# Kernel optimization log

Measured on AMD Instinct MI355X. Metric: run time of the kernel, lower is better.

Reference implementation:

```python
import jax, jax.numpy as jnp
import numpy as np

NUM_HEADS = 16

def _rope(t, cos, sin):
    # t: [B,H,T,hd]; cos/sin: [T,half]
    half = t.shape[-1] // 2
    t1, t2 = t[..., :half], t[..., half:]
    return jnp.concatenate((t1 * cos - t2 * sin, t1 * sin + t2 * cos), axis=-1)

def setup_inputs() -> dict:
    key = jax.random.key(0)
    ks = jax.random.split(key, 5)
    B, T, D = 2, 2048, 2048
    s = 0.02
    return {
        'x': jax.random.normal(ks[0], (B, T, D), jnp.float32),
        'w_qkv': jax.random.normal(ks[1], (3 * D, D), jnp.float32) * s,
        'b_qkv': jax.random.normal(ks[2], (3 * D,), jnp.float32) * s,
        'w_out': jax.random.normal(ks[3], (D, D), jnp.float32) * s,
        'b_out': jax.random.normal(ks[4], (D,), jnp.float32) * s,
    }

def reference(x, w_qkv, b_qkv, w_out, b_out):
    B, T, D = x.shape
    H = NUM_HEADS
    hd = D // H
    half = hd // 2
    # fused QKV projection (torch Linear: x @ W^T + b)
    qkv = (x @ w_qkv.T + b_qkv).reshape(B, T, H, 3, hd)
    q, k, v = qkv[..., 0, :], qkv[..., 1, :], qkv[..., 2, :]
    q, k, v = (jnp.transpose(t, (0, 2, 1, 3)) for t in (q, k, v))  # [B,H,T,hd]
    # RoPE frequencies (buffer computed as in __init__)
    theta = 1.0 / (10000.0 ** (jnp.arange(half, dtype=jnp.float32) / half))
    freq = jnp.arange(T, dtype=jnp.float32)[:, None] * theta[None, :]  # [T,half]
    cos, sin = jnp.cos(freq), jnp.sin(freq)
    q = _rope(q, cos, sin)
    k = _rope(k, cos, sin)
    # causal attention; NOTE: source scales by embed_dim**-0.5
    scale = D ** (-0.5)
    scores = jnp.einsum('bhqd,bhkd->bhqk', q, k) * scale
    mask = jnp.triu(jnp.full((T, T), -1e9, dtype=scores.dtype), k=1)
    weights = jax.nn.softmax(scores + mask, axis=-1)
    attn = jnp.einsum('bhqk,bhkd->bhqd', weights, v)
    attn = jnp.transpose(attn, (0, 2, 1, 3)).reshape(B, T, D)
    return attn @ w_out.T + b_out
```

## Files before the change

kernel.cpp:

```cpp
#include <hip/hip_runtime.h>
#include <math.h>

#define NHEAD 16
#define TSEQ  2048
#define BATCH 2
#define DM    2048

typedef __attribute__((ext_vector_type(8))) short bf16x8;
typedef __attribute__((ext_vector_type(4))) float f32x4;

__device__ __forceinline__ short f2bf(float f) {
    unsigned u = __builtin_bit_cast(unsigned, f);
    u += 0x7fff + ((u >> 16) & 1);
    return (short)(u >> 16);
}
__device__ __forceinline__ float bf2f(short s) {
    unsigned u = ((unsigned)(unsigned short)s) << 16;
    return __builtin_bit_cast(float, u);
}
__device__ __forceinline__ void gload_lds16(const void* g, void* l) {
    __builtin_amdgcn_global_load_lds(
        (const __attribute__((address_space(1))) unsigned int*)g,
        (__attribute__((address_space(3))) unsigned int*)l, 16, 0, 0);
}

__global__ __launch_bounds__(256)
void cast_all(const float* __restrict__ x, short* __restrict__ xb,
              const float* __restrict__ wq, short* __restrict__ wqb,
              const float* __restrict__ wo, short* __restrict__ wob)
{
    int bid = blockIdx.x;
    const float* src; short* dst; int lb;
    if (bid < 4096)       { src = x;  dst = xb;  lb = bid; }
    else if (bid < 10240) { src = wq; dst = wqb; lb = bid - 4096; }
    else                  { src = wo; dst = wob; lb = bid - 10240; }
    int i = (lb * 256 + threadIdx.x) * 8;
    float4 a = *(const float4*)(src + i);
    float4 b = *(const float4*)(src + i + 4);
    bf16x8 o;
    o[0]=f2bf(a.x); o[1]=f2bf(a.y); o[2]=f2bf(a.z); o[3]=f2bf(a.w);
    o[4]=f2bf(b.x); o[5]=f2bf(b.y); o[6]=f2bf(b.z); o[7]=f2bf(b.w);
    *(bf16x8*)(dst + i) = o;
}

#define BARRIER() __builtin_amdgcn_s_barrier()
#define WAIT_LGKM0() do { asm volatile("s_waitcnt lgkmcnt(0)" ::: "memory"); \
                          __builtin_amdgcn_sched_barrier(0); } while (0)
#define WAIT_VM(N) asm volatile("s_waitcnt vmcnt(" #N ")" ::: "memory")

#define LOAD_A(BUF, MH) do {                                                  \
    const short* base_ = sm + (BUF)*32768 + (MH)*8192;                        \
    _Pragma("unroll")                                                         \
    for (int m_ = 0; m_ < 4; ++m_) {                                          \
        int j_ = wr*64 + m_*16 + lane15;                                      \
        const short* rp_ = base_ + j_*64;                                     \
        int sw_ = (j_ & 7) << 3;                                              \
        af[m_][0] = *(const bf16x8*)(rp_ + ((quad << 3) ^ sw_));              \
        af[m_][1] = *(const bf16x8*)(rp_ + ((32 + (quad << 3)) ^ sw_));       \
    }                                                                         \
} while (0)

#define LOAD_B(BUF, NH, BB) do {                                              \
    const short* base_ = sm + (BUF)*32768 + 16384 + (NH)*8192;                \
    _Pragma("unroll")                                                         \
    for (int n_ = 0; n_ < 2; ++n_) {                                          \
        int j_ = wc*32 + n_*16 + lane15;                                      \
        const short* rp_ = base_ + j_*64;                                     \
        int sw_ = (j_ & 7) << 3;                                              \
        BB[n_][0] = *(const bf16x8*)(rp_ + ((quad << 3) ^ sw_));              \
        BB[n_][1] = *(const bf16x8*)(rp_ + ((32 + (quad << 3)) ^ sw_));       \
    }                                                                         \
} while (0)

#define STAGE_A(T, MH) do { if ((T) < 32) {                                   \
    short* dst_ = sm + (((T) & 1) << 15) + ((MH) << 13);                      \
    const int kt_ = (T) << 6;                                                 \
    _Pragma("unroll")                                                         \
    for (int i_ = 0; i_ < 2; ++i_) {                                          \
        int ci_ = i_*512 + tid;                                               \
        int j_ = ci_ >> 3, lc_ = ci_ & 7;                                     \
        int r_ = (j_ & 63) + ((j_ >> 6) << 7) + (MH)*64;                      \
        gload_lds16(A + (size_t)(row0 + r_)*2048 + kt_ + ((lc_ ^ (j_ & 7)) << 3), \
                    dst_ + ci_*8);                                            \
    } } } while (0)

#define STAGE_B(T, NH) do { if ((T) < 32) {                                   \
    short* dst_ = sm + (((T) & 1) << 15) + 16384 + ((NH) << 13);              \
    const int kt_ = (T) << 6;                                                 \
    _Pragma("unroll")                                                         \
    for (int i_ = 0; i_ < 2; ++i_) {                                          \
        int ci_ = i_*512 + tid;                                               \
        int j_ = ci_ >> 3, lc_ = ci_ & 7;                                     \
        int r_ = (j_ & 31) + ((j_ >> 5) << 6) + (NH)*32;                      \
        gload_lds16(W + (size_t)(col0 + r_)*2048 + kt_ + ((lc_ ^ (j_ & 7)) << 3), \
                    dst_ + ci_*8);                                            \
    } } } while (0)

#define MMA_Q(MH, NH, BB) do {                                                \
    _Pragma("unroll")                                                         \
    for (int m_ = 0; m_ < 4; ++m_) {                                          \
        _Pragma("unroll")                                                     \
        for (int n_ = 0; n_ < 2; ++n_) {                                      \
            f32x4 c_ = acc[(MH)*4 + m_][(NH)*2 + n_];                         \
            c_ = __builtin_amdgcn_mfma_f32_16x16x32_bf16(af[m_][0], BB[n_][0], c_, 0, 0, 0); \
            c_ = __builtin_amdgcn_mfma_f32_16x16x32_bf16(af[m_][1], BB[n_][1], c_, 0, 0, 0); \
            acc[(MH)*4 + m_][(NH)*2 + n_] = c_;                               \
        }                                                                     \
    }                                                                         \
} while (0)

__global__ __launch_bounds__(512, 2)
void gemm_qkv_rope(const short* __restrict__ A, const short* __restrict__ W,
                   const float* __restrict__ bias, short* __restrict__ qfrag,
                   short* __restrict__ kfrag, short* __restrict__ vfrag)
{
    __shared__ short sm[65536];
    const int tid = threadIdx.x;
    const int lane = tid & 63, w = tid >> 6;
    const int lane15 = lane & 15, quad = lane >> 4;
    const int wr = w >> 2, wc = w & 3;
    const int row0 = blockIdx.y * 256, col0 = blockIdx.x * 256;

    f32x4 acc[8][4];
    #pragma unroll
    for (int mi = 0; mi < 8; ++mi)
        #pragma unroll
        for (int ni = 0; ni < 4; ++ni)
            acc[mi][ni] = (f32x4){0.f, 0.f, 0.f, 0.f};

    bf16x8 af[4][2], bb0[2][2], bb1[2][2];

    STAGE_A(0, 0); STAGE_B(0, 0); STAGE_A(0, 1); STAGE_B(0, 1);
    STAGE_A(1, 0); STAGE_B(1, 0); STAGE_A(1, 1); STAGE_B(1, 1);
    WAIT_VM(8);
    BARRIER();

    for (int i = 0; i < 16; ++i) {
        const int ta = 2*i + 2;
        const int tb = 2*i + 3;
        LOAD_A(0, 0);
        LOAD_B(0, 0, bb0);
        BARRIER(); WAIT_LGKM0();
        __builtin_amdgcn_s_setprio(1); MMA_Q(0, 0, bb0); __builtin_amdgcn_s_setprio(0);
        BARRIER();
        LOAD_B(0, 1, bb1);
        STAGE_A(ta, 0); STAGE_B(ta, 0);
        BARRIER(); WAIT_LGKM0();
        __builtin_amdgcn_s_setprio(1); MMA_Q(0, 1, bb1); __builtin_amdgcn_s_setprio(0);
        BARRIER();
        LOAD_A(0, 1);
        STAGE_B(ta, 1);
        BARRIER(); WAIT_LGKM0();
        __builtin_amdgcn_s_setprio(1); MMA_Q(1, 1, bb1); __builtin_amdgcn_s_setprio(0);
        BARRIER();
        STAGE_A(ta, 1);
        if (i == 15) { WAIT_VM(0); } else { WAIT_VM(8); }
        BARRIER();
        __builtin_amdgcn_s_setprio(1); MMA_Q(1, 0, bb0); __builtin_amdgcn_s_setprio(0);
        BARRIER();
        LOAD_A(1, 0);
        LOAD_B(1, 0, bb0);
        BARRIER(); WAIT_LGKM0();
        __builtin_amdgcn_s_setprio(1); MMA_Q(0, 0, bb0); __builtin_amdgcn_s_setprio(0);
        BARRIER();
        LOAD_B(1, 1, bb1);
        STAGE_A(tb, 0); STAGE_B(tb, 0);
        BARRIER(); WAIT_LGKM0();
        __builtin_amdgcn_s_setprio(1); MMA_Q(0, 1, bb1); __builtin_amdgcn_s_setprio(0);
        BARRIER();
        LOAD_A(1, 1);
        STAGE_B(tb, 1);
        BARRIER(); WAIT_LGKM0();
        __builtin_amdgcn_s_setprio(1); MMA_Q(1, 1, bb1); __builtin_amdgcn_s_setprio(0);
        BARRIER();
        STAGE_A(tb, 1);
        if (i < 15) { WAIT_VM(8); }
        BARRIER();
        __builtin_amdgcn_s_setprio(1); MMA_Q(1, 0, bb0); __builtin_amdgcn_s_setprio(0);
        BARRIER();
    }

    const int b = row0 >> 11;
    const int t0g = row0 & 2047;
    #pragma unroll
    for (int ch = 0; ch < 2; ++ch) {
        const int cidx = (col0 >> 7) + ch;
        const int head = cidx / 3, type = cidx % 3;
        __syncthreads();
        if ((wc >> 1) == ch) {
            #pragma unroll
            for (int ni = 0; ni < 4; ++ni) {
                int d = (wc & 1)*64 + ni*16 + lane15;
                float bv = bias[col0 + ch*128 + d];
                #pragma unroll
                for (int mi = 0; mi < 8; ++mi) {
                    int rowb = wr*128 + mi*16 + quad*4;
                    #pragma unroll
                    for (int r = 0; r < 4; ++r)
                        sm[(rowb + r)*136 + d] = f2bf(acc[mi][ni][r] + bv);
                }
            }
        }
        __syncthreads();
        if (type < 2) {
            const float sc = (type == 0) ? 0.022097086912079608f : 1.0f;
            short* dst = (type == 0 ? qfrag : kfrag) + (size_t)(b*NHEAD + head)*262144;
            #pragma unroll
            for (int it = 0; it < 4; ++it) {
                int c = it*512 + tid;
                int l15 = c & 15, q_ = (c >> 4) & 3, kc = (c >> 6) & 1, rowhi = c >> 7;
                int lrow = rowhi*16 + l15;
                int t = t0g + lrow;
                bf16x8 a8 = *(const bf16x8*)(sm + lrow*136 + kc*32 + q_*8);
                bf16x8 b8 = *(const bf16x8*)(sm + lrow*136 + kc*32 + q_*8 + 64);
                bf16x8 oa, ob;
                #pragma unroll
                for (int j = 0; j < 8; ++j) {
                    int d = kc*32 + q_*8 + j;
                    float trev = exp2f(-(float)d * (13.287712379549449f / 64.0f))
                                 * 0.15915494309189535f;
                    float ang = (float)t * trev;
                    float fr = ang - floorf(ang);
                    float sn, cs;
                    __sincosf(fr * 6.283185307179586f, &sn, &cs);
                    float va = bf2f(a8[j]), vb = bf2f(b8[j]);
                    oa[j] = f2bf((va*cs - vb*sn)*sc);
                    ob[j] = f2bf((va*sn + vb*cs)*sc);
                }
                size_t base = (size_t)((t0g >> 4) + rowhi)*2048 + (q_*16 + l15)*8;
                *(bf16x8*)(dst + base + kc*512)        = oa;
                *(bf16x8*)(dst + base + kc*512 + 1024) = ob;
            }
        } else {
            short* dst = vfrag + (size_t)(b*NHEAD + head)*262144;
            #pragma unroll
            for (int it = 0; it < 8; ++it) {
                int c = it*512 + tid;
                int lane_ = c & 63, rest = c >> 6;
                int q_ = lane_ >> 4, l15 = lane_ & 15;
                int dt = rest & 7, kc2 = (rest >> 3) & 1, kbt = rest >> 4;
                int d = dt*16 + l15;
                bf16x8 v;
                #pragma unroll
                for (int j = 0; j < 8; ++j)
                    v[j] = sm[(kbt*64 + kc2*32 + q_*8 + j)*136 + d];
                *(bf16x8*)(dst + (size_t)((t0g >> 6) + kbt)*8192
                            + dt*1024 + kc2*512 + lane_*8) = v;
            }
        }
    }
}

__global__ __launch_bounds__(256)
void gemm_out(const short* __restrict__ A, const short* __restrict__ W,
              const float* __restrict__ bias, float* __restrict__ Cout,
              int N, int K)
{
    __shared__ short As[128 * 64];
    __shared__ short Bs[128 * 64];
    const int tid = threadIdx.x;
    const int lane = tid & 63, w = tid >> 6;
    const int lane15 = lane & 15, quad = lane >> 4;
    const int wr = w >> 1, wc = w & 1;
    const int row0 = blockIdx.y * 128, col0 = blockIdx.x * 128;

    f32x4 acc[4][4];
    #pragma unroll
    for (int mi = 0; mi < 4; ++mi)
        #pragma unroll
        for (int ni = 0; ni < 4; ++ni)
            acc[mi][ni] = (f32x4){0.f, 0.f, 0.f, 0.f};

    for (int kt = 0; kt < K; kt += 64) {
        __syncthreads();
        #pragma unroll
        for (int i = 0; i < 4; ++i) {
            int ci = i * 256 + tid;
            int row = ci >> 3, lc = ci & 7;
            int gc = lc ^ (row & 7);
            gload_lds16(A + (size_t)(row0 + row) * K + kt + gc * 8, As + ci * 8);
            gload_lds16(W + (size_t)(col0 + row) * K + kt + gc * 8, Bs + ci * 8);
        }
        __syncthreads();
        #pragma unroll
        for (int kc = 0; kc < 2; ++kc) {
            bf16x8 af[4], bfr[4];
            #pragma unroll
            for (int mi = 0; mi < 4; ++mi) {
                int r = wr * 64 + mi * 16 + lane15;
                af[mi] = *(const bf16x8*)(As + r * 64 + ((kc * 4 + quad) ^ (r & 7)) * 8);
            }
            #pragma unroll
            for (int ni = 0; ni < 4; ++ni) {
                int r = wc * 64 + ni * 16 + lane15;
                bfr[ni] = *(const bf16x8*)(Bs + r * 64 + ((kc * 4 + quad) ^ (r & 7)) * 8);
            }
            #pragma unroll
            for (int mi = 0; mi < 4; ++mi)
                #pragma unroll
                for (int ni = 0; ni < 4; ++ni)
                    acc[mi][ni] = __builtin_amdgcn_mfma_f32_16x16x32_bf16(
                        af[mi], bfr[ni], acc[mi][ni], 0, 0, 0);
        }
    }

    #pragma unroll
    for (int mi = 0; mi < 4; ++mi)
        #pragma unroll
        for (int ni = 0; ni < 4; ++ni) {
            int col = col0 + wc * 64 + ni * 16 + lane15;
            float bv = bias[col];
            #pragma unroll
            for (int r = 0; r < 4; ++r) {
                int row = row0 + wr * 64 + mi * 16 + quad * 4 + r;
                Cout[(size_t)row * N + col] = acc[mi][ni][r] + bv;
            }
        }
}

__global__ __launch_bounds__(256)
void attn3(const short* __restrict__ qfrag, const short* __restrict__ kfrag,
           const short* __restrict__ vfrag, short* __restrict__ attnb)
{
    __shared__ short KV[2][16384];
    __shared__ short Pb[4][1152];
    const int tid = threadIdx.x;
    const int lane = tid & 63, w = tid >> 6;
    const int lane15 = lane & 15, quad = lane >> 4;
    const int g = (blockIdx.x + blockIdx.y) & 15;
    const int qb = blockIdx.z ? (15 - g) : g;
    const int h = blockIdx.y, b = blockIdx.z;
    const int bh = b * NHEAD + h;
    const int q0 = qb * 128;
    short* Pw = Pb[w];

    bf16x8 qf[2][4];
    {
        const short* qp = qfrag + (size_t)bh * 262144
                        + (size_t)(qb * 8 + w * 2) * 2048 + lane * 8;
        #pragma unroll
        for (int nq = 0; nq < 2; ++nq)
            #pragma unroll
            for (int kc = 0; kc < 4; ++kc)
                qf[nq][kc] = *(const bf16x8*)(qp + nq * 2048 + kc * 512);
    }

    f32x4 acc[8][2];
    #pragma unroll
    for (int dt = 0; dt < 8; ++dt)
        #pragma unroll
        for (int nq = 0; nq < 2; ++nq)
            acc[dt][nq] = (f32x4){0.f, 0.f, 0.f, 0.f};
    float m_s[2] = {-3e38f, -3e38f}, l_s[2] = {0.f, 0.f};

    const short* kf_src = kfrag + (size_t)bh * 262144;
    const short* vf_src = vfrag + (size_t)bh * 262144;
    const int kb_max = 2 * qb + 1;
    const int qtop = q0 + w * 32 + 31;
    const int diag0 = (q0 + w * 32) >> 6;

    #pragma unroll
    for (int i = 0; i < 4; ++i) {
        int ci = i * 256 + tid;
        gload_lds16(kf_src + ci * 8, KV[0] + ci * 8);
        gload_lds16(vf_src + ci * 8, KV[0] + 8192 + ci * 8);
    }

    for (int kb = 0; kb <= kb_max; ++kb) {
        __syncthreads();
        if (kb < kb_max) {
            const short* ks = kf_src + (size_t)(kb + 1) * 8192;
            const short* vs = vf_src + (size_t)(kb + 1) * 8192;
            short* kd = KV[(kb + 1) & 1];
            #pragma unroll
            for (int i = 0; i < 4; ++i) {
                int ci = i * 256 + tid;
                gload_lds16(ks + ci * 8, kd + ci * 8);
                gload_lds16(vs + ci * 8, kd + 8192 + ci * 8);
            }
        }
        if (kb * 64 > qtop) continue;
        const short* Ks = KV[kb & 1];
        const short* Vs = Ks + 8192;

        f32x4 st[2][4];
        #pragma unroll
        for (int nq = 0; nq < 2; ++nq)
            #pragma unroll
            for (int mi = 0; mi < 4; ++mi)
                st[nq][mi] = (f32x4){0.f, 0.f, 0.f, 0.f};
        #pragma unroll
        for (int mi = 0; mi < 4; ++mi) {
            bf16x8 kf4[4];
            #pragma unroll
            for (int kc = 0; kc < 4; ++kc)
                kf4[kc] = *(const bf16x8*)(Ks + ((mi * 4 + kc) * 64 + lane) * 8);
            #pragma unroll
            for (int kc = 0; kc < 4; ++kc)
                #pragma unroll
                for (int nq = 0; nq < 2; ++nq)
                    st[nq][mi] = __builtin_amdgcn_mfma_f32_16x16x32_bf16(
                        kf4[kc], qf[nq][kc], st[nq][mi], 0, 0, 0);
        }

        if (kb >= diag0) {
            #pragma unroll
            for (int nq = 0; nq < 2; ++nq) {
                int qg = q0 + w * 32 + nq * 16 + lane15;
                #pragma unroll
                for (int mi = 0; mi < 4; ++mi)
                    #pragma unroll
                    for (int r = 0; r < 4; ++r)
                        if (kb * 64 + mi * 16 + quad * 4 + r > qg)
                            st[nq][mi][r] = -3e38f;
            }
        }

        bf16x8 pb[2][2];
        #pragma unroll
        for (int nq = 0; nq < 2; ++nq) {
            float mt = st[nq][0][0];
            #pragma unroll
            for (int mi = 0; mi < 4; ++mi)
                #pragma unroll
                for (int r = 0; r < 4; ++r)
                    mt = fmaxf(mt, st[nq][mi][r]);
            mt = fmaxf(mt, __shfl_xor(mt, 16));
            mt = fmaxf(mt, __shfl_xor(mt, 32));
            float mn = fmaxf(m_s[nq], mt);
            float alpha = __expf(m_s[nq] - mn);
            m_s[nq] = mn;
            float sum = 0.f;
            #pragma unroll
            for (int mi = 0; mi < 4; ++mi)
                #pragma unroll
                for (int r = 0; r < 4; ++r) {
                    float p = __expf(st[nq][mi][r] - mn);
                    st[nq][mi][r] = p;
                    sum += p;
                }
            sum += __shfl_xor(sum, 16);
            sum += __shfl_xor(sum, 32);
            l_s[nq] = l_s[nq] * alpha + sum;
            #pragma unroll
            for (int dt = 0; dt < 8; ++dt) {
                acc[dt][nq][0] *= alpha; acc[dt][nq][1] *= alpha;
                acc[dt][nq][2] *= alpha; acc[dt][nq][3] *= alpha;
            }
            short* pr = Pw + lane15 * 72 + quad * 4;
            #pragma unroll
            for (int mi = 0; mi < 4; ++mi) {
                unsigned lo = (unsigned)(unsigned short)f2bf(st[nq][mi][0])
                            | ((unsigned)(unsigned short)f2bf(st[nq][mi][1]) << 16);
                unsigned hi = (unsigned)(unsigned short)f2bf(st[nq][mi][2])
                            | ((unsigned)(unsigned short)f2bf(st[nq][mi][3]) << 16);
                *(unsigned*)(pr + mi * 16)     = lo;
                *(unsigned*)(pr + mi * 16 + 2) = hi;
            }
            __asm__ volatile("s_waitcnt lgkmcnt(0)" ::: "memory");
            #pragma unroll
            for (int kc2 = 0; kc2 < 2; ++kc2)
                pb[nq][kc2] = *(const bf16x8*)(Pw + lane15 * 72 + kc2 * 32 + quad * 8);
            __asm__ volatile("s_waitcnt lgkmcnt(0)" ::: "memory");
        }

        #pragma unroll
        for (int dt = 0; dt < 8; ++dt)
            #pragma unroll
            for (int kc2 = 0; kc2 < 2; ++kc2) {
                bf16x8 vf = *(const bf16x8*)(Vs + ((dt * 2 + kc2) * 64 + lane) * 8);
                #pragma unroll
                for (int nq = 0; nq < 2; ++nq)
                    acc[dt][nq] = __builtin_amdgcn_mfma_f32_16x16x32_bf16(
                        vf, pb[nq][kc2], acc[dt][nq], 0, 0, 0);
            }
    }

    __syncthreads();
    short* Eb = KV[0];
    #pragma unroll
    for (int nq = 0; nq < 2; ++nq) {
        float inv = 1.f / l_s[nq];
        int qrow = w * 32 + nq * 16 + lane15;
        #pragma unroll
        for (int dt = 0; dt < 8; ++dt) {
            unsigned lo = (unsigned)(unsigned short)f2bf(acc[dt][nq][0] * inv)
                        | ((unsigned)(unsigned short)f2bf(acc[dt][nq][1] * inv) << 16);
            unsigned hi = (unsigned)(unsigned short)f2bf(acc[dt][nq][2] * inv)
                        | ((unsigned)(unsigned short)f2bf(acc[dt][nq][3] * inv) << 16);
            *(unsigned*)(Eb + qrow * 136 + dt * 16 + quad * 4)     = lo;
            *(unsigned*)(Eb + qrow * 136 + dt * 16 + quad * 4 + 2) = hi;
        }
    }
    __syncthreads();
    {
        int r = tid >> 1, half = tid & 1;
        short* orow = attnb + (size_t)(b * TSEQ + q0 + r) * DM + h * 128 + half * 64;
        #pragma unroll
        for (int i = 0; i < 8; ++i)
            *(bf16x8*)(orow + i * 8) =
                *(const bf16x8*)(Eb + r * 136 + half * 64 + i * 8);
    }
}

extern "C" void kernel_launch(void* const* d_in, const int* in_sizes, int n_in,
                              void* d_out, int out_size, void* d_ws, size_t ws_size,
                              hipStream_t stream)
{
    const float* x     = (const float*)d_in[0];
    const float* w_qkv = (const float*)d_in[1];
    const float* b_qkv = (const float*)d_in[2];
    const float* w_out = (const float*)d_in[3];
    const float* b_out = (const float*)d_in[4];
    float* out = (float*)d_out;

    char* ws = (char*)d_ws;
    short* xb    = (short*)(ws);
    short* wqkvb = (short*)(ws + 16777216);
    short* woutb = (short*)(ws + 41943040);
    short* qfrag = (short*)(ws + 50331648);
    short* kfrag = (short*)(ws + 67108864);
    short* vfrag = (short*)(ws + 83886080);
    short* attnb = xb;

    cast_all<<<12288, 256, 0, stream>>>(x, xb, w_qkv, wqkvb, w_out, woutb);

    {
        dim3 g2(24, 16);
        gemm_qkv_rope<<<g2, 512, 0, stream>>>(xb, wqkvb, b_qkv, qfrag, kfrag, vfrag);
    }
    {
        dim3 g2(16, NHEAD, BATCH);
        attn3<<<g2, 256, 0, stream>>>(qfrag, kfrag, vfrag, attnb);
    }
    {
        dim3 g2(16, 32);
        gemm_out<<<g2, 256, 0, stream>>>(attnb, woutb, b_out, out, 2048, 2048);
    }
}
```

Measured before the change: 381.9 us.

## Read K/V fragments directly from global memory instead of LDS double-buffering

Drops the block-wide LDS double-buffered K/V staging and the per-iteration __syncthreads, so each wave reads K and V fragments straight from global memory. Each wave now loops only up to its own causal end instead of the block's maximum. The P staging buffer gets per-nq slices so both halves are written before a single wait. This cuts LDS footprint and barriers, which may raise occupancy, but it relies on L1/L2 to serve K/V data that four waves previously shared through LDS.

```diff
diff --git a/kernel.cpp b/kernel.cpp
--- a/kernel.cpp
+++ b/kernel.cpp
@@ -322,8 +322,7 @@
 void attn3(const short* __restrict__ qfrag, const short* __restrict__ kfrag,
            const short* __restrict__ vfrag, short* __restrict__ attnb)
 {
-    __shared__ short KV[2][16384];
-    __shared__ short Pb[4][1152];
+    __shared__ short SMEM[17408];
     const int tid = threadIdx.x;
     const int lane = tid & 63, w = tid >> 6;
     const int lane15 = lane & 15, quad = lane >> 4;
@@ -332,7 +331,7 @@
     const int h = blockIdx.y, b = blockIdx.z;
     const int bh = b * NHEAD + h;
     const int q0 = qb * 128;
-    short* Pw = Pb[w];
+    short* Pw = SMEM + w * 2304;
 
     bf16x8 qf[2][4];
     {
@@ -355,33 +354,13 @@
 
     const short* kf_src = kfrag + (size_t)bh * 262144;
     const short* vf_src = vfrag + (size_t)bh * 262144;
-    const int kb_max = 2 * qb + 1;
     const int qtop = q0 + w * 32 + 31;
+    const int kb_end = qtop >> 6;
     const int diag0 = (q0 + w * 32) >> 6;
 
-    #pragma unroll
-    for (int i = 0; i < 4; ++i) {
-        int ci = i * 256 + tid;
-        gload_lds16(kf_src + ci * 8, KV[0] + ci * 8);
-        gload_lds16(vf_src + ci * 8, KV[0] + 8192 + ci * 8);
-    }
-
-    for (int kb = 0; kb <= kb_max; ++kb) {
-        __syncthreads();
-        if (kb < kb_max) {
-            const short* ks = kf_src + (size_t)(kb + 1) * 8192;
-            const short* vs = vf_src + (size_t)(kb + 1) * 8192;
-            short* kd = KV[(kb + 1) & 1];
-            #pragma unroll
-            for (int i = 0; i < 4; ++i) {
-                int ci = i * 256 + tid;
-                gload_lds16(ks + ci * 8, kd + ci * 8);
-                gload_lds16(vs + ci * 8, kd + 8192 + ci * 8);
-            }
-        }
-        if (kb * 64 > qtop) continue;
-        const short* Ks = KV[kb & 1];
-        const short* Vs = Ks + 8192;
+    for (int kb = 0; kb <= kb_end; ++kb) {
+        const short* Ks = kf_src + (size_t)kb * 8192;
+        const short* Vs = vf_src + (size_t)kb * 8192;
 
         f32x4 st[2][4];
         #pragma unroll
@@ -416,7 +395,6 @@
             }
         }
 
-        bf16x8 pb[2][2];
         #pragma unroll
         for (int nq = 0; nq < 2; ++nq) {
             float mt = st[nq][0][0];
@@ -447,7 +425,7 @@
                 acc[dt][nq][0] *= alpha; acc[dt][nq][1] *= alpha;
                 acc[dt][nq][2] *= alpha; acc[dt][nq][3] *= alpha;
             }
-            short* pr = Pw + lane15 * 72 + quad * 4;
+            short* pr = Pw + nq * 1152 + lane15 * 72 + quad * 4;
             #pragma unroll
             for (int mi = 0; mi < 4; ++mi) {
                 unsigned lo = (unsigned)(unsigned short)f2bf(st[nq][mi][0])
@@ -457,12 +435,16 @@
                 *(unsigned*)(pr + mi * 16)     = lo;
                 *(unsigned*)(pr + mi * 16 + 2) = hi;
             }
-            __asm__ volatile("s_waitcnt lgkmcnt(0)" ::: "memory");
+        }
+        __asm__ volatile("s_waitcnt lgkmcnt(0)" ::: "memory");
+        __builtin_amdgcn_sched_barrier(0);
+        bf16x8 pb[2][2];
+        #pragma unroll
+        for (int nq = 0; nq < 2; ++nq)
             #pragma unroll
             for (int kc2 = 0; kc2 < 2; ++kc2)
-                pb[nq][kc2] = *(const bf16x8*)(Pw + lane15 * 72 + kc2 * 32 + quad * 8);
-            __asm__ volatile("s_waitcnt lgkmcnt(0)" ::: "memory");
-        }
+                pb[nq][kc2] = *(const bf16x8*)(Pw + nq * 1152 + lane15 * 72
+                                               + kc2 * 32 + quad * 8);
 
         #pragma unroll
         for (int dt = 0; dt < 8; ++dt)
@@ -477,7 +459,7 @@
     }
 
     __syncthreads();
-    short* Eb = KV[0];
+    short* Eb = SMEM;
     #pragma unroll
     for (int nq = 0; nq < 2; ++nq) {
         float inv = 1.f / l_s[nq];
```

Measured after the change: 484.8 us. 26.9% more time.

## Shrink QKV GEMM tile to 128x256 with triple-buffered LDS pipeline

Applied to the files above, without the earlier changes.

The QKV+RoPE GEMM now uses a 128x256 output tile instead of 256x256, which doubles the grid to 768 blocks and halves the accumulator registers. The main loop is restructured into a simpler per-k-tile schedule with a three-stage LDS ring that prefetches two tiles ahead. The goal is better CU occupancy and load balance and lower register pressure. The cost is lower arithmetic intensity per block, more global and LDS traffic for the weight tile, and larger shared memory use (144KB per block).

```diff
diff --git a/kernel.cpp b/kernel.cpp
--- a/kernel.cpp
+++ b/kernel.cpp
@@ -48,65 +48,44 @@
                           __builtin_amdgcn_sched_barrier(0); } while (0)
 #define WAIT_VM(N) asm volatile("s_waitcnt vmcnt(" #N ")" ::: "memory")
 
-#define LOAD_A(BUF, MH) do {                                                  \
-    const short* base_ = sm + (BUF)*32768 + (MH)*8192;                        \
-    _Pragma("unroll")                                                         \
-    for (int m_ = 0; m_ < 4; ++m_) {                                          \
-        int j_ = wr*64 + m_*16 + lane15;                                      \
-        const short* rp_ = base_ + j_*64;                                     \
-        int sw_ = (j_ & 7) << 3;                                              \
-        af[m_][0] = *(const bf16x8*)(rp_ + ((quad << 3) ^ sw_));              \
-        af[m_][1] = *(const bf16x8*)(rp_ + ((32 + (quad << 3)) ^ sw_));       \
-    }                                                                         \
-} while (0)
-
-#define LOAD_B(BUF, NH, BB) do {                                              \
-    const short* base_ = sm + (BUF)*32768 + 16384 + (NH)*8192;                \
-    _Pragma("unroll")                                                         \
-    for (int n_ = 0; n_ < 2; ++n_) {                                          \
-        int j_ = wc*32 + n_*16 + lane15;                                      \
-        const short* rp_ = base_ + j_*64;                                     \
-        int sw_ = (j_ & 7) << 3;                                              \
-        BB[n_][0] = *(const bf16x8*)(rp_ + ((quad << 3) ^ sw_));              \
-        BB[n_][1] = *(const bf16x8*)(rp_ + ((32 + (quad << 3)) ^ sw_));       \
-    }                                                                         \
-} while (0)
-
-#define STAGE_A(T, MH) do { if ((T) < 32) {                                   \
-    short* dst_ = sm + (((T) & 1) << 15) + ((MH) << 13);                      \
+#define STAGE(T) do { if ((T) < 32) {                                         \
+    short* dst_ = sm + ((T) % 3) * 24576;                                     \
     const int kt_ = (T) << 6;                                                 \
     _Pragma("unroll")                                                         \
     for (int i_ = 0; i_ < 2; ++i_) {                                          \
         int ci_ = i_*512 + tid;                                               \
-        int j_ = ci_ >> 3, lc_ = ci_ & 7;                                     \
-        int r_ = (j_ & 63) + ((j_ >> 6) << 7) + (MH)*64;                      \
-        gload_lds16(A + (size_t)(row0 + r_)*2048 + kt_ + ((lc_ ^ (j_ & 7)) << 3), \
+        int r_ = ci_ >> 3, lc_ = ci_ & 7;                                     \
+        gload_lds16(A + (size_t)(row0 + r_)*2048 + kt_ + ((lc_ ^ (r_ & 7)) << 3), \
                     dst_ + ci_*8);                                            \
+    }                                                                         \
+    _Pragma("unroll")                                                         \
+    for (int i_ = 0; i_ < 4; ++i_) {                                          \
+        int ci_ = i_*512 + tid;                                               \
+        int r_ = ci_ >> 3, lc_ = ci_ & 7;                                     \
+        gload_lds16(W + (size_t)(col0 + r_)*2048 + kt_ + ((lc_ ^ (r_ & 7)) << 3), \
+                    dst_ + 8192 + ci_*8);                                     \
     } } } while (0)
 
-#define STAGE_B(T, NH) do { if ((T) < 32) {                                   \
-    short* dst_ = sm + (((T) & 1) << 15) + 16384 + ((NH) << 13);              \
-    const int kt_ = (T) << 6;                                                 \
-    _Pragma("unroll")                                                         \
-    for (int i_ = 0; i_ < 2; ++i_) {                                          \
-        int ci_ = i_*512 + tid;                                               \
-        int j_ = ci_ >> 3, lc_ = ci_ & 7;                                     \
-        int r_ = (j_ & 31) + ((j_ >> 5) << 6) + (NH)*32;                      \
-        gload_lds16(W + (size_t)(col0 + r_)*2048 + kt_ + ((lc_ ^ (j_ & 7)) << 3), \
-                    dst_ + ci_*8);                                            \
-    } } } while (0)
-
-#define MMA_Q(MH, NH, BB) do {                                                \
+#define LOADRD(Ab, Bb, KC) do {                                               \
     _Pragma("unroll")                                                         \
     for (int m_ = 0; m_ < 4; ++m_) {                                          \
+        int r_ = wr*64 + m_*16 + lane15;                                      \
+        af[m_] = *(const bf16x8*)((Ab) + r_*64 + ((((KC)*4 + quad) ^ (r_ & 7)) << 3)); \
+    }                                                                         \
+    _Pragma("unroll")                                                         \
+    for (int n_ = 0; n_ < 4; ++n_) {                                          \
+        int r_ = wc*64 + n_*16 + lane15;                                      \
+        bb[n_] = *(const bf16x8*)((Bb) + r_*64 + ((((KC)*4 + quad) ^ (r_ & 7)) << 3)); \
+    }                                                                         \
+} while (0)
+
+#define MMA16() do {                                                          \
+    _Pragma("unroll")                                                         \
+    for (int m_ = 0; m_ < 4; ++m_)                                            \
         _Pragma("unroll")                                                     \
-        for (int n_ = 0; n_ < 2; ++n_) {                                      \
-            f32x4 c_ = acc[(MH)*4 + m_][(NH)*2 + n_];                         \
-            c_ = __builtin_amdgcn_mfma_f32_16x16x32_bf16(af[m_][0], BB[n_][0], c_, 0, 0, 0); \
-            c_ = __builtin_amdgcn_mfma_f32_16x16x32_bf16(af[m_][1], BB[n_][1], c_, 0, 0, 0); \
-            acc[(MH)*4 + m_][(NH)*2 + n_] = c_;                               \
-        }                                                                     \
-    }                                                                         \
+        for (int n_ = 0; n_ < 4; ++n_)                                        \
+            acc[m_][n_] = __builtin_amdgcn_mfma_f32_16x16x32_bf16(            \
+                af[m_], bb[n_], acc[m_][n_], 0, 0, 0);                        \
 } while (0)
 
 __global__ __launch_bounds__(512, 2)
@@ -114,69 +93,38 @@
                    const float* __restrict__ bias, short* __restrict__ qfrag,
                    short* __restrict__ kfrag, short* __restrict__ vfrag)
 {
-    __shared__ short sm[65536];
+    __shared__ short sm[73728];
     const int tid = threadIdx.x;
     const int lane = tid & 63, w = tid >> 6;
     const int lane15 = lane & 15, quad = lane >> 4;
     const int wr = w >> 2, wc = w & 3;
-    const int row0 = blockIdx.y * 256, col0 = blockIdx.x * 256;
-
-    f32x4 acc[8][4];
-    #pragma unroll
-    for (int mi = 0; mi < 8; ++mi)
+    const int row0 = blockIdx.y * 128, col0 = blockIdx.x * 256;
+
+    f32x4 acc[4][4];
+    #pragma unroll
+    for (int mi = 0; mi < 4; ++mi)
         #pragma unroll
         for (int ni = 0; ni < 4; ++ni)
             acc[mi][ni] = (f32x4){0.f, 0.f, 0.f, 0.f};
 
-    bf16x8 af[4][2], bb0[2][2], bb1[2][2];
-
-    STAGE_A(0, 0); STAGE_B(0, 0); STAGE_A(0, 1); STAGE_B(0, 1);
-    STAGE_A(1, 0); STAGE_B(1, 0); STAGE_A(1, 1); STAGE_B(1, 1);
-    WAIT_VM(8);
+    bf16x8 af[4], bb[4];
+
+    STAGE(0); STAGE(1);
+    WAIT_VM(6);
     BARRIER();
 
-    for (int i = 0; i < 16; ++i) {
-        const int ta = 2*i + 2;
-        const int tb = 2*i + 3;
-        LOAD_A(0, 0);
-        LOAD_B(0, 0, bb0);
+    for (int t = 0; t < 32; ++t) {
+        short* Ab = sm + (t % 3) * 24576;
+        short* Bb = Ab + 8192;
+        LOADRD(Ab, Bb, 0);
+        STAGE(t + 2);
         BARRIER(); WAIT_LGKM0();
-        __builtin_amdgcn_s_setprio(1); MMA_Q(0, 0, bb0); __builtin_amdgcn_s_setprio(0);
+        __builtin_amdgcn_s_setprio(1); MMA16(); __builtin_amdgcn_s_setprio(0);
         BARRIER();
-        LOAD_B(0, 1, bb1);
-        STAGE_A(ta, 0); STAGE_B(ta, 0);
+        LOADRD(Ab, Bb, 1);
+        if (t < 30) { WAIT_VM(6); } else { WAIT_VM(0); }
         BARRIER(); WAIT_LGKM0();
-        __builtin_amdgcn_s_setprio(1); MMA_Q(0, 1, bb1); __builtin_amdgcn_s_setprio(0);
-        BARRIER();
-        LOAD_A(0, 1);
-        STAGE_B(ta, 1);
-        BARRIER(); WAIT_LGKM0();
-        __builtin_amdgcn_s_setprio(1); MMA_Q(1, 1, bb1); __builtin_amdgcn_s_setprio(0);
-        BARRIER();
-        STAGE_A(ta, 1);
-        if (i == 15) { WAIT_VM(0); } else { WAIT_VM(8); }
-        BARRIER();
-        __builtin_amdgcn_s_setprio(1); MMA_Q(1, 0, bb0); __builtin_amdgcn_s_setprio(0);
-        BARRIER();
-        LOAD_A(1, 0);
-        LOAD_B(1, 0, bb0);
-        BARRIER(); WAIT_LGKM0();
-        __builtin_amdgcn_s_setprio(1); MMA_Q(0, 0, bb0); __builtin_amdgcn_s_setprio(0);
-        BARRIER();
-        LOAD_B(1, 1, bb1);
-        STAGE_A(tb, 0); STAGE_B(tb, 0);
-        BARRIER(); WAIT_LGKM0();
-        __builtin_amdgcn_s_setprio(1); MMA_Q(0, 1, bb1); __builtin_amdgcn_s_setprio(0);
-        BARRIER();
-        LOAD_A(1, 1);
-        STAGE_B(tb, 1);
-        BARRIER(); WAIT_LGKM0();
-        __builtin_amdgcn_s_setprio(1); MMA_Q(1, 1, bb1); __builtin_amdgcn_s_setprio(0);
-        BARRIER();
-        STAGE_A(tb, 1);
-        if (i < 15) { WAIT_VM(8); }
-        BARRIER();
-        __builtin_amdgcn_s_setprio(1); MMA_Q(1, 0, bb0); __builtin_amdgcn_s_setprio(0);
+        __builtin_amdgcn_s_setprio(1); MMA16(); __builtin_amdgcn_s_setprio(0);
         BARRIER();
     }
 
@@ -184,7 +132,7 @@
     const int t0g = row0 & 2047;
     #pragma unroll
     for (int ch = 0; ch < 2; ++ch) {
-        const int cidx = (col0 >> 7) + ch;
+        const int cidx = (blockIdx.x << 1) + ch;
         const int head = cidx / 3, type = cidx % 3;
         __syncthreads();
         if ((wc >> 1) == ch) {
@@ -193,8 +141,8 @@
                 int d = (wc & 1)*64 + ni*16 + lane15;
                 float bv = bias[col0 + ch*128 + d];
                 #pragma unroll
-                for (int mi = 0; mi < 8; ++mi) {
-                    int rowb = wr*128 + mi*16 + quad*4;
+                for (int mi = 0; mi < 4; ++mi) {
+                    int rowb = wr*64 + mi*16 + quad*4;
                     #pragma unroll
                     for (int r = 0; r < 4; ++r)
                         sm[(rowb + r)*136 + d] = f2bf(acc[mi][ni][r] + bv);
@@ -206,7 +154,7 @@
             const float sc = (type == 0) ? 0.022097086912079608f : 1.0f;
             short* dst = (type == 0 ? qfrag : kfrag) + (size_t)(b*NHEAD + head)*262144;
             #pragma unroll
-            for (int it = 0; it < 4; ++it) {
+            for (int it = 0; it < 2; ++it) {
                 int c = it*512 + tid;
                 int l15 = c & 15, q_ = (c >> 4) & 3, kc = (c >> 6) & 1, rowhi = c >> 7;
                 int lrow = rowhi*16 + l15;
@@ -234,7 +182,7 @@
         } else {
             short* dst = vfrag + (size_t)(b*NHEAD + head)*262144;
             #pragma unroll
-            for (int it = 0; it < 8; ++it) {
+            for (int it = 0; it < 4; ++it) {
                 int c = it*512 + tid;
                 int lane_ = c & 63, rest = c >> 6;
                 int q_ = lane_ >> 4, l15 = lane_ & 15;
@@ -526,7 +474,7 @@
     cast_all<<<12288, 256, 0, stream>>>(x, xb, w_qkv, wqkvb, w_out, woutb);
 
     {
-        dim3 g2(24, 16);
+        dim3 g2(24, 32);
         gemm_qkv_rope<<<g2, 512, 0, stream>>>(xb, wqkvb, b_qkv, qfrag, kfrag, vfrag);
     }
     {
```

After: 381.3 us. About the same (-0.2%).
